# Kernel tuning notes

Hardware: AMD Instinct MI355X
Metric: run time of the kernel (lower is better)

## Reference

```python
import jax, jax.numpy as jnp
import numpy as np

I_CH, O_CH = 64, 64
N_NODES, N_EDGES = 20000, 120000


def build_indices(edge_index):
    """Host-side (numpy) replication of the data-dependent index pipeline:
    sort-by-src -> triplets via searchsorted/repeat_interleave -> sort-by-src ->
    prune low-degree half of nodes -> group-by-src (for scatter-mean) -> reindex.
    All shapes depend only on the (constant) int edge_index.
    """
    ei = np.asarray(edge_index)
    ei = ei[:, np.argsort(ei[0], kind='stable')]
    src, tgt = ei[0], ei[1]
    order = np.argsort(tgt, kind='stable')
    stg = tgt[order]
    lb = np.searchsorted(stg, src, side='left')
    ub = np.searchsorted(stg, src, side='right')
    counts = ub - lb
    T = int(counts.sum())
    rep = np.repeat(np.arange(src.shape[0]), counts)
    start = np.cumsum(counts) - counts
    off = np.arange(T) - start[rep]
    hit = order[lb[rep] + off]
    # triplet rows: (SRC[ALL], TGT[ALL], TGT[R])
    tri = np.stack([src[hit], tgt[hit], tgt[rep]])  # [3, T]
    tri = tri[:, np.argsort(tri[0], kind='stable')]
    # remove(): drop edges touching the lowest-degree half of nodes
    deg = np.bincount(tri.ravel())
    low = np.argsort(deg, kind='stable')[: deg.shape[0] // 2]
    keep = np.ones(deg.shape[0], dtype=bool)
    keep[low] = False
    mask = keep[tri[0]] & keep[tri[1]] & keep[tri[2]]
    pos = np.nonzero(mask)[0]
    tri_kept = tri[:, pos]
    # sum(): group kept triplet-edges by source node
    uniq, inv = np.unique(tri_kept[0], return_inverse=True)
    cnt = np.bincount(inv).astype(np.float32)
    # reindex edge_index to compact node ids
    _, new = np.unique(tri_kept, return_inverse=True)
    new_ei = new.reshape(tri_kept.shape).astype(np.int32)
    return tri.astype(np.int32), pos.astype(np.int32), inv.astype(np.int32), int(uniq.shape[0]), cnt, new_ei


def setup_inputs() -> dict:
    key = jax.random.key(0)
    k1, k2, k3, k4 = jax.random.split(key, 4)
    x = jax.random.normal(k1, (N_NODES, I_CH), dtype=jnp.float32)
    edge_index = jax.random.randint(k2, (2, N_EDGES), 0, N_NODES, dtype=jnp.int32)
    # Conv2d(I, O, (3,1)) parameters
    W = 0.05 * jax.random.normal(k3, (O_CH, I_CH, 3, 1), dtype=jnp.float32)
    b = 0.05 * jax.random.normal(k4, (O_CH,), dtype=jnp.float32)
    return {"x": x, "edge_index": edge_index, "W": W, "b": b}


def reference(x, edge_index, W, b):
    tri, pos, inv, U, cnt, new_ei = build_indices(edge_index)
    tri_j = jnp.asarray(tri)
    # gather: INPUT[i,k,t] = x[tri[k,t], i]  -> g is [3, T, I]
    g = x[tri_j]
    # Conv2d(I,O,(3,1)) on [I,3,T] -> [O,1,T]; squeeze the H dim:
    C = jnp.einsum('oik,kti->ot', W[..., 0], g) + b[:, None]  # [O, T]
    Ck = C[:, jnp.asarray(pos)]  # prune edges touching low-degree nodes
    # scatter-mean over destination group (source node of triplet)
    S = jax.ops.segment_sum(Ck.T, jnp.asarray(inv), num_segments=U)  # [U, O]
    x_new = S / jnp.asarray(cnt)[:, None]
    return x_new, jnp.asarray(new_ei)
```

## Files before the change

kernel.cpp:

```cpp
#include <hip/hip_runtime.h>
#include <stdint.h>

typedef uint32_t u32;
typedef unsigned long long u64;

#define LB_TILE 4096
#define OW_TILE 4096
#define RUN 32

#define S_MAXT 1
#define S_DSTAR 2
#define S_NEED 3
#define S_U 5

__global__ void scan_lb(const u32* __restrict__ in, u32* __restrict__ out, int n,
                        u64* __restrict__ desc){
  __shared__ u32 sh[256];
  __shared__ u32 shPrefix;
  int tid=threadIdx.x, t=blockIdx.x;
  int base = t*LB_TILE + tid*16;
  u32 v[16]; u32 s=0;
#pragma unroll
  for(int k=0;k<16;k++){ u32 xv=(base+k<n)?in[base+k]:0u; v[k]=s; s+=xv; }
  sh[tid]=s; __syncthreads();
  for(int o=1;o<256;o<<=1){
    u32 y=(tid>=o)?sh[tid-o]:0u;
    __syncthreads();
    sh[tid]+=y;
    __syncthreads();
  }
  u32 tileEx = (tid==0)?0u:sh[tid-1];
  u32 agg = sh[255];
  if(tid==0){
    u32 prefix=0u;
    if(t==0){
      atomicExch(&desc[0], ((u64)agg<<32)|2ull);
    } else {
      atomicExch(&desc[t], ((u64)agg<<32)|1ull);
      int j=t-1;
      while(true){
        u64 d=atomicAdd(&desc[j],0ull);
        u32 st=(u32)d;
        if(st==0u) continue;
        prefix += (u32)(d>>32);
        if(st==2u) break;
        --j;
      }
      atomicExch(&desc[t], ((u64)(prefix+agg)<<32)|2ull);
    }
    shPrefix=prefix;
  }
  __syncthreads();
  u32 p=shPrefix+tileEx;
#pragma unroll
  for(int k=0;k<16;k++){ if(base+k<n) out[base+k]=p+v[k]; }
}

__global__ __launch_bounds__(256) void ow32(const u32* __restrict__ in,
    u32* __restrict__ outk, const u32* __restrict__ gbase, u64* __restrict__ desc,
    int shift, int n){
  __shared__ u32 hist[256], bd[256], cnt2[256];
  __shared__ u32 cnt4[4][256];
  int tid=threadIdx.x, b=blockIdx.x, w=tid>>6, lane=tid&63;
  int base=b*OW_TILE;
  hist[tid]=0u; cnt2[tid]=0u;
  cnt4[0][tid]=0u; cnt4[1][tid]=0u; cnt4[2][tid]=0u; cnt4[3][tid]=0u;
  __syncthreads();
  u32 k[16]; bool act[16];
#pragma unroll
  for(int i=0;i<16;i++){
    int p=base+i*256+tid; act[i]=(p<n);
    k[i]=act[i]?in[p]:0u;
    if(act[i]) atomicAdd(&hist[(k[i]>>shift)&255u],1u);
  }
  __syncthreads();
  u32 agg=hist[tid];
  if(b==0){
    atomicExch(&desc[tid], ((u64)agg<<32)|2ull);
    bd[tid]=gbase[tid];
  } else {
    atomicExch(&desc[(size_t)b*256+tid], ((u64)agg<<32)|1ull);
    u32 pre=0u; int j=b-1;
    while(true){
      u64 d=atomicAdd(&desc[(size_t)j*256+tid],0ull);
      u32 st=(u32)d;
      if(st==0u) continue;
      pre+=(u32)(d>>32);
      if(st==2u) break;
      --j;
    }
    atomicExch(&desc[(size_t)b*256+tid], ((u64)(pre+agg)<<32)|2ull);
    bd[tid]=gbase[tid]+pre;
  }
  __syncthreads();
#pragma unroll
  for(int i=0;i<16;i++){
    u32 dig=(k[i]>>shift)&255u;
    u64 m=__ballot(act[i]?1:0);
    for(int bb=0;bb<8;bb++){
      u64 bl=__ballot((int)((dig>>bb)&1u));
      m &= ((dig>>bb)&1u)?bl:~bl;
    }
    u32 rb=(u32)__popcll(m&((1ull<<lane)-1ull));
    if(act[i]&&rb==0u) cnt4[w][dig]=(u32)__popcll(m);
    __syncthreads();
    if(act[i]){
      u32 off=cnt2[dig]+rb;
      for(int w2=0;w2<w;w2++) off+=cnt4[w2][dig];
      u32 pos=bd[dig]+off;
      if(pos<(u32)n) outk[pos]=k[i];
    }
    __syncthreads();
    cnt2[tid]+=cnt4[0][tid]+cnt4[1][tid]+cnt4[2][tid]+cnt4[3][tid];
    cnt4[0][tid]=0u; cnt4[1][tid]=0u; cnt4[2][tid]=0u; cnt4[3][tid]=0u;
    __syncthreads();
  }
}

__global__ __launch_bounds__(256) void ow64(const u64* __restrict__ in,
    u64* __restrict__ outk, const u32* __restrict__ gbase, u64* __restrict__ desc,
    int shift, const u32* __restrict__ dCount, int cap){
  __shared__ u32 hist[256], bd[256], cnt2[256];
  __shared__ u32 cnt4[4][256];
  int n=(int)((*dCount)<(u32)cap?(*dCount):(u32)cap);
  int tid=threadIdx.x, b=blockIdx.x, w=tid>>6, lane=tid&63;
  int base=b*OW_TILE;
  hist[tid]=0u; cnt2[tid]=0u;
  cnt4[0][tid]=0u; cnt4[1][tid]=0u; cnt4[2][tid]=0u; cnt4[3][tid]=0u;
  __syncthreads();
  u64 k[16]; bool act[16];
#pragma unroll
  for(int i=0;i<16;i++){
    int p=base+i*256+tid; act[i]=(p<n);
    k[i]=act[i]?in[p]:0ull;
    if(act[i]) atomicAdd(&hist[(u32)(k[i]>>shift)&255u],1u);
  }
  __syncthreads();
  u32 agg=hist[tid];
  if(b==0){
    atomicExch(&desc[tid], ((u64)agg<<32)|2ull);
    bd[tid]=gbase[tid];
  } else {
    atomicExch(&desc[(size_t)b*256+tid], ((u64)agg<<32)|1ull);
    u32 pre=0u; int j=b-1;
    while(true){
      u64 d=atomicAdd(&desc[(size_t)j*256+tid],0ull);
      u32 st=(u32)d;
      if(st==0u) continue;
      pre+=(u32)(d>>32);
      if(st==2u) break;
      --j;
    }
    atomicExch(&desc[(size_t)b*256+tid], ((u64)(pre+agg)<<32)|2ull);
    bd[tid]=gbase[tid]+pre;
  }
  __syncthreads();
#pragma unroll
  for(int i=0;i<16;i++){
    u32 dig=(u32)(k[i]>>shift)&255u;
    u64 m=__ballot(act[i]?1:0);
    for(int bb=0;bb<8;bb++){
      u64 bl=__ballot((int)((dig>>bb)&1u));
      m &= ((dig>>bb)&1u)?bl:~bl;
    }
    u32 rb=(u32)__popcll(m&((1ull<<lane)-1ull));
    if(act[i]&&rb==0u) cnt4[w][dig]=(u32)__popcll(m);
    __syncthreads();
    if(act[i]){
      u32 off=cnt2[dig]+rb;
      for(int w2=0;w2<w;w2++) off+=cnt4[w2][dig];
      u32 pos=bd[dig]+off;
      if(pos<(u32)n) outk[pos]=k[i];
    }
    __syncthreads();
    cnt2[tid]+=cnt4[0][tid]+cnt4[1][tid]+cnt4[2][tid]+cnt4[3][tid];
    cnt4[0][tid]=0u; cnt4[1][tid]=0u; cnt4[2][tid]=0u; cnt4[3][tid]=0u;
    __syncthreads();
  }
}

__global__ void k_edge0(const u32* __restrict__ src, const u32* __restrict__ tgt,
                        u32* cntS, u32* cntT, u32* keyA, int E){
  int j=blockIdx.x*256+threadIdx.x;
  if(j>=E) return;
  u32 s=src[j], t=tgt[j];
  atomicAdd(&cntS[s],1u); atomicAdd(&cntT[t],1u);
  keyA[j]=(s<<16)|t;
}

__global__ void k_deg2m(const u32* __restrict__ src, const u32* __restrict__ tgt,
                        const u32* __restrict__ cntS, const u32* __restrict__ cntT,
                        u32* deg, int* scal, int E){
  __shared__ int mx;
  if(threadIdx.x==0) mx=-1;
  __syncthreads();
  int e=blockIdx.x*256+threadIdx.x;
  int loc=-1;
  if(e<E){
    u32 s=src[e], t=tgt[e];
    u32 w0=cntS[t], w2=cntT[s];
    if(w0){ atomicAdd(&deg[s],w0); loc=(int)(s>t?s:t); }
    if(w2){ atomicAdd(&deg[t],w2); if((int)t>loc) loc=(int)t; }
  }
  if(loc>=0) atomicMax(&mx,loc);
  __syncthreads();
  if(threadIdx.x==0 && mx>=0) atomicMax(&scal[S_MAXT],mx);
}

__global__ void k_degNodeHist(const u32* __restrict__ cntS, const u32* __restrict__ cntT,
                              u32* deg, u32* dh, int NN, const int* __restrict__ scal){
  int v=blockIdx.x*256+threadIdx.x;
  if(v>=NN) return;
  u32 d=deg[v]+cntS[v]*cntT[v];
  deg[v]=d;
  if(v<=scal[S_MAXT]){ if(d>65535u)d=65535u; atomicAdd(&dh[d],1u); }
}

__global__ void k_dstar1b(const u32* __restrict__ dh, int* scal){
  __shared__ u32 part[256];
  __shared__ u32 sc[256];
  int t=threadIdx.x;
  long long kk=(((long long)scal[S_MAXT])+1)>>1;
  u32 s=0;
  for(int i=0;i<256;i++) s+=dh[t*256+i];
  part[t]=s; sc[t]=s; __syncthreads();
  for(int o=1;o<256;o<<=1){
    u32 y=(t>=o)?sc[t-o]:0u; __syncthreads();
    sc[t]+=y; __syncthreads();
  }
  if(kk==0){ if(t==0){ scal[S_DSTAR]=-1; scal[S_NEED]=0; } return; }
  long long cum=(long long)(sc[t]-part[t]);
  if(kk-1>=cum && kk-1<cum+(long long)part[t]){
    long long c=cum;
    for(int i=0;i<256;i++){
      u32 h=dh[t*256+i];
      if(kk-1>=c && kk-1<c+(long long)h){ scal[S_DSTAR]=t*256+i; scal[S_NEED]=(int)(kk-c); break; }
      c+=h;
    }
  }
}

__global__ void k_ef(const u32* __restrict__ deg, u32* ef, int NN, const int* __restrict__ scal){
  int v=blockIdx.x*256+threadIdx.x;
  if(v>NN) return;
  ef[v] = (v<NN && v<=scal[S_MAXT] && (int)deg[v]==scal[S_DSTAR]) ? 1u:0u;
}

__global__ void k_keep(const u32* __restrict__ deg, const u32* __restrict__ rankEq,
                       u32* keep, int NN, const int* __restrict__ scal){
  int v=blockIdx.x*256+threadIdx.x;
  if(v>=NN) return;
  int d=(int)deg[v]; int ds=scal[S_DSTAR]; int need=scal[S_NEED];
  u32 kp=1u;
  if(d<ds) kp=0u;
  else if(d==ds && (int)rankEq[v]<need) kp=0u;
  keep[v]=kp;
}

__global__ void k_keptCnt(const u32* __restrict__ src, const u32* __restrict__ tgt,
                          const u32* __restrict__ keep, u32* kc, int E){
  int j=blockIdx.x*256+threadIdx.x;
  if(j<E && keep[src[j]]) atomicAdd(&kc[tgt[j]],1u);
}

__global__ void k_gbase4(const u32* __restrict__ cntS, const u32* __restrict__ cntT,
                         u32* __restrict__ gbase, int NN){
  __shared__ u32 sh[256];
  int p=blockIdx.x, d=threadIdx.x;
  const u32* c=(p<2)?cntS:cntT;
  u32 s=0;
  if((p&1)==0){ for(int i=d;i<NN;i+=256) s+=c[i]; }
  else { int s0=d*256, s1=s0+256; if(s1>NN)s1=NN; for(int i=s0;i<s1;i++) s+=c[i]; }
  sh[d]=s; __syncthreads();
  for(int o=1;o<256;o<<=1){
    u32 y=(d>=o)?sh[d-o]:0u; __syncthreads();
    sh[d]+=y; __syncthreads();
  }
  gbase[p*256+d]=sh[d]-s;
}

__global__ void k_scan256(const u32* __restrict__ hg, u32* __restrict__ gb, int H){
  __shared__ u32 sh[256];
  int t=threadIdx.x;
  for(int hh=0;hh<H;hh++){
    u32 v=hg[hh*256+t];
    sh[t]=v; __syncthreads();
    for(int o=1;o<256;o<<=1){
      u32 y=(t>=o)?sh[t-o]:0u; __syncthreads();
      sh[t]+=y; __syncthreads();
    }
    gb[hh*256+t]=sh[t]-v;
    __syncthreads();
  }
}

__global__ void k_cntk(const u32* __restrict__ C, const u32* __restrict__ keep,
                       const u32* __restrict__ keptCnt, u32* cntk, int E){
  int e=blockIdx.x*256+threadIdx.x;
  if(e>E) return;
  if(e==E){ cntk[e]=0u; return; }
  u32 ke=C[e];
  u32 s=ke>>16, te=ke&0xFFFFu;
  cntk[e]=(keep[s]&keep[te])?keptCnt[s]:0u;
}

__global__ void k_gen_trik(const u32* __restrict__ C, const u32* __restrict__ H,
    const u32* __restrict__ rp, const u32* __restrict__ keep,
    const u32* __restrict__ startk, u64* __restrict__ trig, u32* __restrict__ histGT,
    int E, int cap){
  __shared__ u32 h0[256], h1[256];
  int tid=threadIdx.x;
  h0[tid]=0u; h1[tid]=0u;
  __syncthreads();
  int e=blockIdx.x*256+tid;
  if(e<E){
    u32 c0=startk[e], c1=startk[e+1];
    if(c0<c1){
      u32 ke=C[e];
      u32 s=ke>>16, te=ke&0xFFFFu;
      u32 r0=rp[0];
      u32 lb=rp[s]-r0, ub=rp[s+1]-r0;
      u32 idx=c0;
      for(u32 i=lb;i<ub&&idx<c1;++i){
        u32 hsv=H[i]>>16;
        if(keep[hsv]){
          if(idx<(u32)cap){
            u64 key=((u64)hsv<<30)|((u64)s<<15)|(u64)te;
            trig[idx]=key;
            atomicAdd(&h0[(u32)(key>>30)&255u],1u);
            atomicAdd(&h1[(u32)(key>>38)&255u],1u);
          }
          ++idx;
        }
      }
    }
  }
  __syncthreads();
  if(h0[tid]) atomicAdd(&histGT[tid],h0[tid]);
  if(h1[tid]) atomicAdd(&histGT[256+tid],h1[tid]);
}

__global__ void k_heads_present(const u64* __restrict__ tri, u32* __restrict__ hf,
    u32* __restrict__ present, const u32* __restrict__ dCount, int KC){
  int Tk=(int)((*dCount)<(u32)KC?(*dCount):(u32)KC);
  int q=blockIdx.x*256+threadIdx.x;
  if(q>KC) return;
  u32 f=0u;
  if(q<Tk){
    u64 key=tri[q];
    f=(q==0||(key>>30)!=(tri[q-1]>>30))?1u:0u;
    present[key>>30]=1u;
    present[(key>>15)&0x7FFFu]=1u;
    present[key&0x7FFFu]=1u;
  }
  hf[q]=f;
}

__global__ void k_gs_ei(const u64* __restrict__ tri, const u32* __restrict__ hf,
    const u32* __restrict__ hsAll, u32* __restrict__ gs, float* __restrict__ out,
    int* scal, const u32* __restrict__ dCount, int KC, int out_size){
  int Tk=(int)((*dCount)<(u32)KC?(*dCount):(u32)KC);
  u32 U=hsAll[KC+1];
  int q=blockIdx.x*256+threadIdx.x;
  if(q==0){ scal[S_U]=(int)U; gs[U]=(u32)Tk; }
  if(q>=Tk) return;
  if(hf[q]) gs[hsAll[q+1]-1u]=(u32)q;
  u64 key=tri[q];
  int bs=(int)U*64;
  int i0=bs+q, i1=bs+Tk+q, i2=bs+2*Tk+q;
  if(i0<out_size) out[i0]=(float)(hsAll[(size_t)KC+1+(size_t)(key>>30)]-U);
  if(i1<out_size) out[i1]=(float)(hsAll[(size_t)KC+1+(size_t)((key>>15)&0x7FFFu)]-U);
  if(i2<out_size) out[i2]=(float)(hsAll[(size_t)KC+1+(size_t)(key&0x7FFFu)]-U);
}

__global__ __launch_bounds__(256) void k_xsum(const float* __restrict__ x,
    const u64* __restrict__ tri, const u32* __restrict__ hs,
    float* __restrict__ S1, float* __restrict__ S2,
    const u32* __restrict__ dCount, int KC){
  int Tk=(int)((*dCount)<(u32)KC?(*dCount):(u32)KC);
  int w=threadIdx.x>>6, lane=threadIdx.x&63;
  int r=blockIdx.x*4+w;
  int q0=r*RUN; if(q0>=Tk) return;
  int q1=q0+RUN; if(q1>Tk)q1=Tk;
  int gcur=(int)hs[q0+1]-1;
  float a1=0.f,a2=0.f;
  for(int q=q0;q<q1;q++){
    int g=(int)hs[q+1]-1;
    if(g!=gcur){
      atomicAdd(&S1[(size_t)gcur*64+lane],a1);
      atomicAdd(&S2[(size_t)gcur*64+lane],a2);
      a1=0.f;a2=0.f;gcur=g;
    }
    u64 key=tri[q];
    a1+=x[(size_t)((key>>15)&0x7FFFull)*64+lane];
    a2+=x[(size_t)(key&0x7FFFull)*64+lane];
  }
  atomicAdd(&S1[(size_t)gcur*64+lane],a1);
  atomicAdd(&S2[(size_t)gcur*64+lane],a2);
}

__global__ __launch_bounds__(256) void k_xmat(const float* __restrict__ x,
    const float* __restrict__ W, const float* __restrict__ b,
    const u64* __restrict__ tri, const u32* __restrict__ gs,
    const float* __restrict__ S1, const float* __restrict__ S2,
    float* __restrict__ out, const int* __restrict__ scal){
  __shared__ float Wl[192*65];
  __shared__ float sv[4][192];
  int tid=threadIdx.x;
  for(int j=tid;j<12288;j+=256){
    int r=j%192, o=j/192;
    Wl[r*65+o]=W[j];
  }
  __syncthreads();
  int U=scal[S_U];
  int w=tid>>6, lane=tid&63;
  float bv=b[lane];
  for(int g=blockIdx.x*4+w; g<U; g+=gridDim.x*4){
    u32 q0=gs[g], q1=gs[g+1];
    u32 uniq=(u32)(tri[q0]>>30);
    sv[w][lane]=x[(size_t)uniq*64+lane];
    sv[w][64+lane]=S1[(size_t)g*64+lane];
    sv[w][128+lane]=S2[(size_t)g*64+lane];
    float acc0=0.f, acc12=0.f;
#pragma unroll 4
    for(int ii=0;ii<64;ii++){
      acc0  += Wl[(ii*3+0)*65+lane]*sv[w][ii];
      acc12 += Wl[(ii*3+1)*65+lane]*sv[w][64+ii]
             + Wl[(ii*3+2)*65+lane]*sv[w][128+ii];
    }
    out[(size_t)g*64+lane] = bv + acc0 + acc12/(float)(q1-q0);
  }
}

extern "C" void kernel_launch(void* const* d_in, const int* in_sizes, int n_in,
                              void* d_out, int out_size, void* d_ws, size_t ws_size,
                              hipStream_t stream){
  const float* x = (const float*)d_in[0];
  const int*   ei = (const int*)d_in[1];
  const float* W = (const float*)d_in[2];
  const float* b = (const float*)d_in[3];
  int NN = in_sizes[0]/64;
  int E  = in_sizes[1]/2;
  const u32* src=(const u32*)ei;
  const u32* tgt=(const u32*)(ei+E);

  int KC = ((out_size/3 + OW_TILE-1)/OW_TILE)*OW_TILE; if(KC<OW_TILE) KC=OW_TILE;
  int B_E=(E+OW_TILE-1)/OW_TILE;
  int B_T=KC/OW_TILE;

  char* base=(char*)d_ws; size_t off=0;
  auto alloc=[&](size_t nInts)->u32*{
    u32* p=(u32*)(base+off);
    off += ( (nInts*4 + 255) & ~(size_t)255 );
    return p;
  };
  int* scal=(int*)alloc(64);
  u32* cntS=alloc(NN);
  u32* deg=alloc(NN); u32* degHist=alloc(65536);
  u32* keptCnt=alloc(NN);
  u32* histGT=alloc(2*256);
  u32* catA=alloc(2*(size_t)(NN+1));
  u64* descS=(u64*)alloc(2*1024);
  u64* descE=(u64*)alloc(2*(size_t)(4*B_E*256));
  u64* descT=(u64*)alloc(2*(size_t)(2*B_T*256));
  u32* hfp=alloc((size_t)KC+1+NN+1);
  float* S1=(float*)alloc((size_t)NN*64);
  float* S2=(float*)alloc((size_t)NN*64);
  size_t zoneBytes = off;
  u32* ebA=alloc(E); u32* ebB=alloc(E); u32* ebC=alloc(E);
  u64* triA=(u64*)alloc(2*(size_t)KC); u64* triB=(u64*)alloc(2*(size_t)KC);
  u32* cntk=alloc(E+1); u32* startk=alloc(E+1);
  u32* catB=alloc(2*(size_t)(NN+1));
  u32* gbaseE=alloc(4*256); u32* gbaseT=alloc(2*256);
  u32* keep=alloc(NN);
  u32* gs=alloc(NN+2);
  u32* hsAll=alloc((size_t)KC+1+NN+1);
  if(off > ws_size) return;

  u32* ef=catA; u32* cntT=catA+(NN+1);
  u32* rankEq=catB; u32* rp=catB+(NN+1);
  u32* hf=hfp; u32* present=hfp+(KC+1);
  const u32* dCount=startk+E;

  size_t descUsed=0;
  auto scan_ex=[&](const u32* in, u32* out, int n){
    int nb=(n+LB_TILE-1)/LB_TILE;
    scan_lb<<<nb,256,0,stream>>>(in,out,n,descS+descUsed);
    descUsed += (size_t)nb;
  };

  int gE=(E+255)/256, gE1=(E+256)/256;
  int gNN=(NN+255)/256, gNN1=(NN+256)/256;
  int gKC=(KC+255)/256, gKC1=(KC+256)/256;

  hipMemsetAsync(base,0,zoneBytes,stream);

  k_edge0<<<gE,256,0,stream>>>(src,tgt,cntS,cntT,ebA,E);
  k_deg2m<<<gE,256,0,stream>>>(src,tgt,cntS,cntT,deg,scal,E);
  k_degNodeHist<<<gNN,256,0,stream>>>(cntS,cntT,deg,degHist,NN,scal);
  k_dstar1b<<<1,256,0,stream>>>(degHist,scal);
  k_ef<<<gNN1,256,0,stream>>>(deg,ef,NN,scal);
  scan_ex(catA,catB,2*(NN+1));
  k_keep<<<gNN,256,0,stream>>>(deg,rankEq,keep,NN,scal);
  k_keptCnt<<<gE,256,0,stream>>>(src,tgt,keep,keptCnt,E);

  k_gbase4<<<4,256,0,stream>>>(cntS,cntT,gbaseE,NN);
  ow32<<<B_E,256,0,stream>>>(ebA,ebB,gbaseE+0*256,descE+(size_t)0*B_E*256,16,E);
  ow32<<<B_E,256,0,stream>>>(ebB,ebC,gbaseE+1*256,descE+(size_t)1*B_E*256,24,E);
  ow32<<<B_E,256,0,stream>>>(ebC,ebA,gbaseE+2*256,descE+(size_t)2*B_E*256,0,E);
  ow32<<<B_E,256,0,stream>>>(ebA,ebB,gbaseE+3*256,descE+(size_t)3*B_E*256,8,E);

  k_cntk<<<gE1,256,0,stream>>>(ebC,keep,keptCnt,cntk,E);
  scan_ex(cntk,startk,E+1);
  k_gen_trik<<<gE,256,0,stream>>>(ebC,ebB,rp,keep,startk,triA,histGT,E,KC);

  k_scan256<<<1,256,0,stream>>>(histGT,gbaseT,2);
  ow64<<<B_T,256,0,stream>>>(triA,triB,gbaseT+0*256,descT+(size_t)0*B_T*256,30,dCount,KC);
  ow64<<<B_T,256,0,stream>>>(triB,triA,gbaseT+1*256,descT+(size_t)1*B_T*256,38,dCount,KC);

  k_heads_present<<<gKC1,256,0,stream>>>(triA,hf,present,dCount,KC);
  scan_ex(hfp,hsAll,KC+1+NN+1);
  float* outF=(float*)d_out;
  k_gs_ei<<<gKC,256,0,stream>>>(triA,hf,hsAll,gs,outF,scal,dCount,KC,out_size);

  k_xsum<<<KC/(4*RUN),256,0,stream>>>(x,triA,hsAll,S1,S2,dCount,KC);
  k_xmat<<<768,256,0,stream>>>(x,W,b,triA,gs,S1,S2,outF,scal);
}
```

Before: 373.1 us.

## Compact kept-source edges before tgt-sort and shrink onesweep tiles

Edges are now compacted by kept source before the last two radix passes on the target key, so those passes and the triplet generation only touch kept edges. k_gen_trik no longer scans and filters the full adjacency range per edge. The per-edge offsets are built from a combined three-array scan. Onesweep tile sizes drop from 4096 to 1024 (edges) and 2048 (triplets) for more blocks and shorter decoupled-lookback chains. The cost is an extra scan and a compaction kernel, plus more lookback descriptors from the smaller tiles.

After: 345.7 us. 1.08x faster.

```diff
diff --git a/kernel.cpp b/kernel.cpp
--- a/kernel.cpp
+++ b/kernel.cpp
@@ -5,13 +5,12 @@
 typedef unsigned long long u64;
 
 #define LB_TILE 4096
-#define OW_TILE 4096
-#define RUN 32
 
 #define S_MAXT 1
 #define S_DSTAR 2
 #define S_NEED 3
 #define S_U 5
+#define S_EK 6
 
 __global__ void scan_lb(const u32* __restrict__ in, u32* __restrict__ out, int n,
                         u64* __restrict__ desc){
@@ -56,19 +55,21 @@
   for(int k=0;k<16;k++){ if(base+k<n) out[base+k]=p+v[k]; }
 }
 
-__global__ __launch_bounds__(256) void ow32(const u32* __restrict__ in,
+template<int ROUNDS>
+__global__ __launch_bounds__(256) void ow32k(const u32* __restrict__ in,
     u32* __restrict__ outk, const u32* __restrict__ gbase, u64* __restrict__ desc,
-    int shift, int n){
+    int shift, int hostN, const u32* __restrict__ devN, int cap){
   __shared__ u32 hist[256], bd[256], cnt2[256];
   __shared__ u32 cnt4[4][256];
+  int n = (hostN>=0)?hostN:(int)((*devN)<(u32)cap?(*devN):(u32)cap);
   int tid=threadIdx.x, b=blockIdx.x, w=tid>>6, lane=tid&63;
-  int base=b*OW_TILE;
+  int base=b*ROUNDS*256;
   hist[tid]=0u; cnt2[tid]=0u;
   cnt4[0][tid]=0u; cnt4[1][tid]=0u; cnt4[2][tid]=0u; cnt4[3][tid]=0u;
   __syncthreads();
-  u32 k[16]; bool act[16];
+  u32 k[ROUNDS]; bool act[ROUNDS];
 #pragma unroll
-  for(int i=0;i<16;i++){
+  for(int i=0;i<ROUNDS;i++){
     int p=base+i*256+tid; act[i]=(p<n);
     k[i]=act[i]?in[p]:0u;
     if(act[i]) atomicAdd(&hist[(k[i]>>shift)&255u],1u);
@@ -94,7 +95,7 @@
   }
   __syncthreads();
 #pragma unroll
-  for(int i=0;i<16;i++){
+  for(int i=0;i<ROUNDS;i++){
     u32 dig=(k[i]>>shift)&255u;
     u64 m=__ballot(act[i]?1:0);
     for(int bb=0;bb<8;bb++){
@@ -117,20 +118,21 @@
   }
 }
 
-__global__ __launch_bounds__(256) void ow64(const u64* __restrict__ in,
+template<int ROUNDS>
+__global__ __launch_bounds__(256) void ow64k(const u64* __restrict__ in,
     u64* __restrict__ outk, const u32* __restrict__ gbase, u64* __restrict__ desc,
-    int shift, const u32* __restrict__ dCount, int cap){
+    int shift, const u32* __restrict__ devN, int cap){
   __shared__ u32 hist[256], bd[256], cnt2[256];
   __shared__ u32 cnt4[4][256];
-  int n=(int)((*dCount)<(u32)cap?(*dCount):(u32)cap);
+  int n=(int)((*devN)<(u32)cap?(*devN):(u32)cap);
   int tid=threadIdx.x, b=blockIdx.x, w=tid>>6, lane=tid&63;
-  int base=b*OW_TILE;
+  int base=b*ROUNDS*256;
   hist[tid]=0u; cnt2[tid]=0u;
   cnt4[0][tid]=0u; cnt4[1][tid]=0u; cnt4[2][tid]=0u; cnt4[3][tid]=0u;
   __syncthreads();
-  u64 k[16]; bool act[16];
+  u64 k[ROUNDS]; bool act[ROUNDS];
 #pragma unroll
-  for(int i=0;i<16;i++){
+  for(int i=0;i<ROUNDS;i++){
     int p=base+i*256+tid; act[i]=(p<n);
     k[i]=act[i]?in[p]:0ull;
     if(act[i]) atomicAdd(&hist[(u32)(k[i]>>shift)&255u],1u);
@@ -156,7 +158,7 @@
   }
   __syncthreads();
 #pragma unroll
-  for(int i=0;i<16;i++){
+  for(int i=0;i<ROUNDS;i++){
     u32 dig=(u32)(k[i]>>shift)&255u;
     u64 m=__ballot(act[i]?1:0);
     for(int bb=0;bb<8;bb++){
@@ -247,7 +249,8 @@
 }
 
 __global__ void k_keep(const u32* __restrict__ deg, const u32* __restrict__ rankEq,
-                       u32* keep, int NN, const int* __restrict__ scal){
+                       const u32* __restrict__ cntS, u32* keep, u32* kcsSeg,
+                       int NN, const int* __restrict__ scal){
   int v=blockIdx.x*256+threadIdx.x;
   if(v>=NN) return;
   int d=(int)deg[v]; int ds=scal[S_DSTAR]; int need=scal[S_NEED];
@@ -255,6 +258,7 @@
   if(d<ds) kp=0u;
   else if(d==ds && (int)rankEq[v]<need) kp=0u;
   keep[v]=kp;
+  kcsSeg[v]=kp*cntS[v];
 }
 
 __global__ void k_keptCnt(const u32* __restrict__ src, const u32* __restrict__ tgt,
@@ -263,11 +267,11 @@
   if(j<E && keep[src[j]]) atomicAdd(&kc[tgt[j]],1u);
 }
 
-__global__ void k_gbase4(const u32* __restrict__ cntS, const u32* __restrict__ cntT,
-                         u32* __restrict__ gbase, int NN){
+__global__ void k_gbase4(const u32* __restrict__ cntS, const u32* __restrict__ keptCnt,
+                         u32* __restrict__ gbase, int NN, int* scal){
   __shared__ u32 sh[256];
   int p=blockIdx.x, d=threadIdx.x;
-  const u32* c=(p<2)?cntS:cntT;
+  const u32* c=(p<2)?cntS:keptCnt;
   u32 s=0;
   if((p&1)==0){ for(int i=d;i<NN;i+=256) s+=c[i]; }
   else { int s0=d*256, s1=s0+256; if(s1>NN)s1=NN; for(int i=s0;i<s1;i++) s+=c[i]; }
@@ -277,6 +281,7 @@
     sh[d]+=y; __syncthreads();
   }
   gbase[p*256+d]=sh[d]-s;
+  if(p==3 && d==255) scal[S_EK]=(int)sh[255];
 }
 
 __global__ void k_scan256(const u32* __restrict__ hg, u32* __restrict__ gb, int H){
@@ -294,20 +299,26 @@
   }
 }
 
-__global__ void k_cntk(const u32* __restrict__ C, const u32* __restrict__ keep,
-                       const u32* __restrict__ keptCnt, u32* cntk, int E){
+__global__ void k_cntkCompact(const u32* __restrict__ C, const u32* __restrict__ keep,
+    const u32* __restrict__ keptCnt, const u32* __restrict__ cat3out,
+    u32* cntk, u32* __restrict__ H2, int E, int NN1){
   int e=blockIdx.x*256+threadIdx.x;
   if(e>E) return;
   if(e==E){ cntk[e]=0u; return; }
   u32 ke=C[e];
   u32 s=ke>>16, te=ke&0xFFFFu;
-  cntk[e]=(keep[s]&keep[te])?keptCnt[s]:0u;
+  u32 ks=keep[s];
+  cntk[e]=(ks&keep[te])?keptCnt[s]:0u;
+  if(ks){
+    u32 rpS=cat3out[s];
+    u32 kcum=cat3out[NN1+s]-(u32)E;
+    H2[kcum+((u32)e-rpS)]=ke;
+  }
 }
 
 __global__ void k_gen_trik(const u32* __restrict__ C, const u32* __restrict__ H,
-    const u32* __restrict__ rp, const u32* __restrict__ keep,
-    const u32* __restrict__ startk, u64* __restrict__ trig, u32* __restrict__ histGT,
-    int E, int cap){
+    const u32* __restrict__ rpk, const u32* __restrict__ startk,
+    u64* __restrict__ trig, u32* __restrict__ histGT, int E, int cap){
   __shared__ u32 h0[256], h1[256];
   int tid=threadIdx.x;
   h0[tid]=0u; h1[tid]=0u;
@@ -318,19 +329,17 @@
     if(c0<c1){
       u32 ke=C[e];
       u32 s=ke>>16, te=ke&0xFFFFu;
-      u32 r0=rp[0];
-      u32 lb=rp[s]-r0, ub=rp[s+1]-r0;
-      u32 idx=c0;
-      for(u32 i=lb;i<ub&&idx<c1;++i){
-        u32 hsv=H[i]>>16;
-        if(keep[hsv]){
-          if(idx<(u32)cap){
-            u64 key=((u64)hsv<<30)|((u64)s<<15)|(u64)te;
-            trig[idx]=key;
-            atomicAdd(&h0[(u32)(key>>30)&255u],1u);
-            atomicAdd(&h1[(u32)(key>>38)&255u],1u);
-          }
-          ++idx;
+      u32 r0=rpk[0];
+      u32 lb=rpk[s]-r0;
+      u32 cnt=c1-c0;
+      for(u32 o=0;o<cnt;++o){
+        u32 idx=c0+o;
+        if(idx<(u32)cap){
+          u32 hsv=H[lb+o]>>16;
+          u64 key=((u64)hsv<<30)|((u64)s<<15)|(u64)te;
+          trig[idx]=key;
+          atomicAdd(&h0[(u32)(key>>30)&255u],1u);
+          atomicAdd(&h1[(u32)(key>>38)&255u],1u);
         }
       }
     }
@@ -373,6 +382,7 @@
   if(i2<out_size) out[i2]=(float)(hsAll[(size_t)KC+1+(size_t)(key&0x7FFFu)]-U);
 }
 
+#define RUN 32
 __global__ __launch_bounds__(256) void k_xsum(const float* __restrict__ x,
     const u64* __restrict__ tri, const u32* __restrict__ hs,
     float* __restrict__ S1, float* __restrict__ S2,
@@ -441,12 +451,14 @@
   const float* b = (const float*)d_in[3];
   int NN = in_sizes[0]/64;
   int E  = in_sizes[1]/2;
+  int NN1 = NN+1;
   const u32* src=(const u32*)ei;
   const u32* tgt=(const u32*)(ei+E);
 
-  int KC = ((out_size/3 + OW_TILE-1)/OW_TILE)*OW_TILE; if(KC<OW_TILE) KC=OW_TILE;
-  int B_E=(E+OW_TILE-1)/OW_TILE;
-  int B_T=KC/OW_TILE;
+  const int TE=1024, TT=2048;
+  int KC = ((out_size/3 + TT-1)/TT)*TT; if(KC<TT) KC=TT;
+  int B_E=(E+TE-1)/TE;
+  int B_T=KC/TT;
 
   char* base=(char*)d_ws; size_t off=0;
   auto alloc=[&](size_t nInts)->u32*{
@@ -455,32 +467,33 @@
     return p;
   };
   int* scal=(int*)alloc(64);
-  u32* cntS=alloc(NN);
+  u32* cat3=alloc(3*(size_t)NN1);
+  u32* cntT=alloc(NN1);
   u32* deg=alloc(NN); u32* degHist=alloc(65536);
-  u32* keptCnt=alloc(NN);
   u32* histGT=alloc(2*256);
-  u32* catA=alloc(2*(size_t)(NN+1));
   u64* descS=(u64*)alloc(2*1024);
   u64* descE=(u64*)alloc(2*(size_t)(4*B_E*256));
   u64* descT=(u64*)alloc(2*(size_t)(2*B_T*256));
-  u32* hfp=alloc((size_t)KC+1+NN+1);
+  u32* hfp=alloc((size_t)KC+1+NN1);
   float* S1=(float*)alloc((size_t)NN*64);
   float* S2=(float*)alloc((size_t)NN*64);
   size_t zoneBytes = off;
   u32* ebA=alloc(E); u32* ebB=alloc(E); u32* ebC=alloc(E);
   u64* triA=(u64*)alloc(2*(size_t)KC); u64* triB=(u64*)alloc(2*(size_t)KC);
   u32* cntk=alloc(E+1); u32* startk=alloc(E+1);
-  u32* catB=alloc(2*(size_t)(NN+1));
+  u32* cat3out=alloc(3*(size_t)NN1);
   u32* gbaseE=alloc(4*256); u32* gbaseT=alloc(2*256);
+  u32* ef=alloc(NN1); u32* rankEq=alloc(NN1);
   u32* keep=alloc(NN);
   u32* gs=alloc(NN+2);
-  u32* hsAll=alloc((size_t)KC+1+NN+1);
+  u32* hsAll=alloc((size_t)KC+1+NN1);
   if(off > ws_size) return;
 
-  u32* ef=catA; u32* cntT=catA+(NN+1);
-  u32* rankEq=catB; u32* rp=catB+(NN+1);
+  u32* cntS=cat3; u32* kcsSeg=cat3+NN1; u32* keptCnt=cat3+2*(size_t)NN1;
+  u32* rpk=cat3out+2*(size_t)NN1;
   u32* hf=hfp; u32* present=hfp+(KC+1);
   const u32* dCount=startk+E;
+  const u32* dEk=(const u32*)&scal[S_EK];
 
   size_t descUsed=0;
   auto scan_ex=[&](const u32* in, u32* out, int n){
@@ -500,26 +513,30 @@
   k_degNodeHist<<<gNN,256,0,stream>>>(cntS,cntT,deg,degHist,NN,scal);
   k_dstar1b<<<1,256,0,stream>>>(degHist,scal);
   k_ef<<<gNN1,256,0,stream>>>(deg,ef,NN,scal);
-  scan_ex(catA,catB,2*(NN+1));
-  k_keep<<<gNN,256,0,stream>>>(deg,rankEq,keep,NN,scal);
+  scan_ex(ef,rankEq,NN1);
+  k_keep<<<gNN,256,0,stream>>>(deg,rankEq,cntS,keep,kcsSeg,NN,scal);
   k_keptCnt<<<gE,256,0,stream>>>(src,tgt,keep,keptCnt,E);
 
-  k_gbase4<<<4,256,0,stream>>>(cntS,cntT,gbaseE,NN);
-  ow32<<<B_E,256,0,stream>>>(ebA,ebB,gbaseE+0*256,descE+(size_t)0*B_E*256,16,E);
-  ow32<<<B_E,256,0,stream>>>(ebB,ebC,gbaseE+1*256,descE+(size_t)1*B_E*256,24,E);
-  ow32<<<B_E,256,0,stream>>>(ebC,ebA,gbaseE+2*256,descE+(size_t)2*B_E*256,0,E);
-  ow32<<<B_E,256,0,stream>>>(ebA,ebB,gbaseE+3*256,descE+(size_t)3*B_E*256,8,E);
-
-  k_cntk<<<gE1,256,0,stream>>>(ebC,keep,keptCnt,cntk,E);
+  scan_ex(cat3,cat3out,3*NN1);
+  k_gbase4<<<4,256,0,stream>>>(cntS,keptCnt,gbaseE,NN,scal);
+
+  ow32k<4><<<B_E,256,0,stream>>>(ebA,ebB,gbaseE+0*256,descE+(size_t)0*B_E*256,16,E,nullptr,0);
+  ow32k<4><<<B_E,256,0,stream>>>(ebB,ebC,gbaseE+1*256,descE+(size_t)1*B_E*256,24,E,nullptr,0);
+
+  k_cntkCompact<<<gE1,256,0,stream>>>(ebC,keep,keptCnt,cat3out,cntk,ebA,E,NN1);
   scan_ex(cntk,startk,E+1);
-  k_gen_trik<<<gE,256,0,stream>>>(ebC,ebB,rp,keep,startk,triA,histGT,E,KC);
+
+  ow32k<4><<<B_E,256,0,stream>>>(ebA,ebB,gbaseE+2*256,descE+(size_t)2*B_E*256,0,-1,dEk,E);
+  ow32k<4><<<B_E,256,0,stream>>>(ebB,ebA,gbaseE+3*256,descE+(size_t)3*B_E*256,8,-1,dEk,E);
+
+  k_gen_trik<<<gE,256,0,stream>>>(ebC,ebA,rpk,startk,triA,histGT,E,KC);
 
   k_scan256<<<1,256,0,stream>>>(histGT,gbaseT,2);
-  ow64<<<B_T,256,0,stream>>>(triA,triB,gbaseT+0*256,descT+(size_t)0*B_T*256,30,dCount,KC);
-  ow64<<<B_T,256,0,stream>>>(triB,triA,gbaseT+1*256,descT+(size_t)1*B_T*256,38,dCount,KC);
+  ow64k<8><<<B_T,256,0,stream>>>(triA,triB,gbaseT+0*256,descT+(size_t)0*B_T*256,30,dCount,KC);
+  ow64k<8><<<B_T,256,0,stream>>>(triB,triA,gbaseT+1*256,descT+(size_t)1*B_T*256,38,dCount,KC);
 
   k_heads_present<<<gKC1,256,0,stream>>>(triA,hf,present,dCount,KC);
-  scan_ex(hfp,hsAll,KC+1+NN+1);
+  scan_ex(hfp,hsAll,KC+1+NN1);
   float* outF=(float*)d_out;
   k_gs_ei<<<gKC,256,0,stream>>>(triA,hf,hsAll,gs,outF,scal,dCount,KC,out_size);
 
```
